# Performance work log

Hardware: AMD Instinct MI355X
Metric: run time of the kernel (lower is better)

## Reference

```python
import jax, jax.numpy as jnp
import numpy as np

S, B, H = 512, 256, 500


def setup_inputs() -> dict:
    key = jax.random.key(0)
    k1, k2, k3, k4, k5 = jax.random.split(key, 5)
    return {
        "hidden": jax.random.normal(k1, (1, B, H), dtype=jnp.float32),
        "encoder_output": jax.random.normal(k2, (S, B, H), dtype=jnp.float32),
        "W_attn": jax.random.normal(k3, (H, 2 * H), dtype=jnp.float32) * 0.02,
        "b_attn": jax.random.normal(k4, (H,), dtype=jnp.float32) * 0.02,
        "v": jax.random.normal(k5, (H,), dtype=jnp.float32),
    }


def reference(hidden, encoder_output, W_attn, b_attn, v):
    # hidden: [1, B, H] -> broadcast to [S, B, H]; concat -> [S, B, 2H]
    s, b, h = encoder_output.shape
    h_exp = jnp.broadcast_to(hidden, (s, b, h))
    cat = jnp.concatenate([h_exp, encoder_output], axis=2)  # [S, B, 2H]
    # Linear(2H -> H) with torch convention W: [out, in], then tanh
    energy = jnp.tanh(jnp.einsum("sbi,hi->sbh", cat, W_attn) + b_attn)  # [S, B, H]
    scores = jnp.einsum("sbh,h->sb", energy, v)  # [S, B]
    attn = jax.nn.softmax(scores.T, axis=1)  # [B, S]
    return attn[:, None, :]  # [B, 1, S]
```

## Files before the change

### kernel.cpp

```cpp
#include <hip/hip_runtime.h>
#include <hip/hip_fp16.h>

#define S_DIM 512
#define B_DIM 256
#define H_DIM 500
#define M_DIM (S_DIM * B_DIM)

typedef _Float16 half8_t __attribute__((ext_vector_type(8)));
typedef float    f32x4  __attribute__((ext_vector_type(4)));

#define WS_W2I 0
#define WS_AT  (512 * 1024)
#define WS_VP  (1024 * 1024)
#define WS_SC  (1024 * 1024 + 4096)

__device__ __forceinline__ void gld_lds16(const void* g, void* l) {
    __builtin_amdgcn_global_load_lds(
        (const __attribute__((address_space(1))) unsigned int*)g,
        (__attribute__((address_space(3))) unsigned int*)l, 16, 0, 0);
}

__global__ void prep_w2_v(const float* __restrict__ W, const float* __restrict__ v,
                          _Float16* __restrict__ W2i, float* __restrict__ vp) {
    int idx = blockIdx.x * blockDim.x + threadIdx.x;
#pragma unroll
    for (int r = 0; r < 2; ++r) {
        int e = idx + r * 131072;
        int n = e >> 9, k = e & 511;
        float val = (n < H_DIM && k < H_DIM) ? W[n * 1000 + 500 + k] : 0.0f;
        int nb = n >> 8, nl = n & 255, ks = k >> 5, ce = (k >> 3) & 3, u = k & 7;
        int cL = ce ^ ((nl >> 1) & 3);
        W2i[((ks * 2 + nb) * 1024 + nl * 4 + cL) * 8 + u] = (_Float16)val;
    }
    if (idx < 512) vp[idx] = (idx < H_DIM) ? v[idx] : 0.0f;
}

__global__ void prep_A(const float* __restrict__ hidden, const float* __restrict__ W,
                       const float* __restrict__ b_attn, float* __restrict__ At) {
    int b = blockIdx.x;
    int t = threadIdx.x;
    __shared__ float hs[512];
    hs[t] = (t < H_DIM) ? hidden[b * H_DIM + t] : 0.0f;
    __syncthreads();
    float acc = 0.0f;
    if (t < H_DIM) {
        acc = b_attn[t];
        const float4* wr = (const float4*)(W + t * 1000);
        const float4* hr = (const float4*)hs;
#pragma unroll 5
        for (int i = 0; i < 125; ++i) {
            float4 w4 = wr[i], h4 = hr[i];
            acc += w4.x * h4.x + w4.y * h4.y + w4.z * h4.z + w4.w * h4.w;
        }
    }
    At[t * B_DIM + b] = acc;
}

__launch_bounds__(512, 4)
__global__ void fused_attn_gemm(const float* __restrict__ enc,
                                const _Float16* __restrict__ W2i,
                                const float* __restrict__ At,
                                const float* __restrict__ vp,
                                float* __restrict__ sct) {
    __shared__ _Float16 As[2][128][32];
    __shared__ _Float16 Bs[2][256][32];
    __shared__ float    red[4][128];

    const int tid  = threadIdx.x;
    const int lane = tid & 63;
    const int wid  = tid >> 6;
    const int wm   = wid >> 2;
    const int wn   = wid & 3;
    const int l15  = lane & 15;
    const int lq   = lane >> 4;

    const int wg    = (blockIdx.x & 7) * 256 + (blockIdx.x >> 3);
    const int mblk  = wg >> 1;
    const int nblk  = wg & 1;
    const int m0    = mblk * 128;
    const int s_idx = mblk >> 1;
    const int bloc  = (mblk & 1) * 128;
    const int n0    = nblk * 256;

    const int r = tid >> 2;
    const int c = tid & 3;
    const float* gA = enc + (size_t)(m0 + r) * H_DIM + c * 8;
    const int ca = (c ^ ((r >> 1) & 3)) * 8;

    const int rch = (lq ^ ((l15 >> 1) & 3)) * 8;

    f32x4 a0, a1;

    auto ldA = [&](int slice) {
        if (slice < 15) {
            a0 = *(const f32x4*)(gA + slice * 32);
            a1 = *(const f32x4*)(gA + slice * 32 + 4);
        } else {
            const float* gr = enc + (size_t)(m0 + r) * H_DIM;
#pragma unroll
            for (int u = 0; u < 4; ++u) {
                int k0 = 480 + c * 8 + u;
                int k1 = k0 + 4;
                a0[u] = (k0 < H_DIM) ? gr[k0] : 0.0f;
                a1[u] = (k1 < H_DIM) ? gr[k1] : 0.0f;
            }
        }
    };
    auto wrA = [&](int buf) {
        half8_t h;
#pragma unroll
        for (int u = 0; u < 4; ++u) { h[u] = (_Float16)a0[u]; h[u + 4] = (_Float16)a1[u]; }
        *(half8_t*)&As[buf][r][ca] = h;
    };
    auto stB = [&](int buf, int ks) {
        const _Float16* pb = W2i + (size_t)(ks * 2 + nblk) * 8192;
        _Float16* dl = (_Float16*)&Bs[buf][0][0] + (size_t)wid * 512;
        gld_lds16(pb + (size_t)tid * 8, dl);
        gld_lds16(pb + (size_t)(tid + 512) * 8, dl + 4096);
    };

    f32x4 acc[4][4];
#pragma unroll
    for (int a = 0; a < 4; ++a)
#pragma unroll
        for (int b = 0; b < 4; ++b) acc[a][b] = 0;

    stB(0, 0);
    ldA(0);
    wrA(0);

    for (int ks = 0; ks < 16; ++ks) {
        const int cur = ks & 1;
        __syncthreads();
        if (ks < 15) {
            stB(cur ^ 1, ks + 1);
            ldA(ks + 1);
        }
        half8_t af[4], bf[4];
#pragma unroll
        for (int mf = 0; mf < 4; ++mf)
            af[mf] = *(const half8_t*)&As[cur][wm * 64 + mf * 16 + l15][rch];
#pragma unroll
        for (int nf = 0; nf < 4; ++nf)
            bf[nf] = *(const half8_t*)&Bs[cur][wn * 64 + nf * 16 + l15][rch];
#pragma unroll
        for (int mf = 0; mf < 4; ++mf)
#pragma unroll
            for (int nf = 0; nf < 4; ++nf)
                acc[mf][nf] = __builtin_amdgcn_mfma_f32_16x16x32_f16(af[mf], bf[nf], acc[mf][nf], 0, 0, 0);
        if (ks < 15) wrA(cur ^ 1);
    }

    float vpv[4];
#pragma unroll
    for (int nf = 0; nf < 4; ++nf) vpv[nf] = vp[n0 + wn * 64 + nf * 16 + l15];

    float pj[4][4];
#pragma unroll
    for (int mf = 0; mf < 4; ++mf)
#pragma unroll
        for (int j = 0; j < 4; ++j) pj[mf][j] = 0.0f;

#pragma unroll
    for (int mf = 0; mf < 4; ++mf) {
#pragma unroll
        for (int nf = 0; nf < 4; ++nf) {
            int h = n0 + wn * 64 + nf * 16 + l15;
            f32x4 av = *(const f32x4*)(At + h * B_DIM + bloc + wm * 64 + mf * 16 + lq * 4);
#pragma unroll
            for (int j = 0; j < 4; ++j) {
                float x  = acc[mf][nf][j] + av[j];
                float xc = fminf(fmaxf(x, -9.0f), 9.0f);
                float e  = __expf(2.0f * xc);
                float th = (e - 1.0f) / (e + 1.0f);
                pj[mf][j] += vpv[nf] * th;
            }
        }
    }

#pragma unroll
    for (int mf = 0; mf < 4; ++mf)
#pragma unroll
        for (int j = 0; j < 4; ++j) {
            float s = pj[mf][j];
            s += __shfl_xor(s, 1); s += __shfl_xor(s, 2);
            s += __shfl_xor(s, 4); s += __shfl_xor(s, 8);
            if (l15 == 0) red[wn][wm * 64 + mf * 16 + lq * 4 + j] = s;
        }
    __syncthreads();
    if (tid < 128) {
        float p = red[0][tid] + red[1][tid] + red[2][tid] + red[3][tid];
        sct[(size_t)nblk * M_DIM + (size_t)(bloc + tid) * S_DIM + s_idx] = p;
    }
}

__global__ void softmax_rows(const float* __restrict__ sct, float* __restrict__ out) {
    int b = blockIdx.x;
    int t = threadIdx.x;
    int lane = t & 63, w = t >> 6;
    size_t idx = (size_t)b * S_DIM + t;
    float v = sct[idx] + sct[idx + M_DIM];
    float m = v;
#pragma unroll
    for (int off = 1; off < 64; off <<= 1) m = fmaxf(m, __shfl_xor(m, off));
    __shared__ float sm[8], ss[8];
    if (lane == 0) sm[w] = m;
    __syncthreads();
    m = sm[0];
#pragma unroll
    for (int i = 1; i < 8; ++i) m = fmaxf(m, sm[i]);
    float e = __expf(v - m);
    float s = e;
#pragma unroll
    for (int off = 1; off < 64; off <<= 1) s += __shfl_xor(s, off);
    if (lane == 0) ss[w] = s;
    __syncthreads();
    s = ss[0];
#pragma unroll
    for (int i = 1; i < 8; ++i) s += ss[i];
    out[(size_t)b * S_DIM + t] = e / s;
}

extern "C" void kernel_launch(void* const* d_in, const int* in_sizes, int n_in,
                              void* d_out, int out_size, void* d_ws, size_t ws_size,
                              hipStream_t stream) {
    const float* hidden = (const float*)d_in[0];
    const float* enc    = (const float*)d_in[1];
    const float* W      = (const float*)d_in[2];
    const float* b_attn = (const float*)d_in[3];
    const float* v      = (const float*)d_in[4];
    float* out = (float*)d_out;

    char* ws = (char*)d_ws;
    _Float16* W2i = (_Float16*)(ws + WS_W2I);
    float*    At  = (float*)(ws + WS_AT);
    float*    vp  = (float*)(ws + WS_VP);
    float*    sct = (float*)(ws + WS_SC);

    prep_w2_v<<<512, 256, 0, stream>>>(W, v, W2i, vp);
    prep_A<<<256, 512, 0, stream>>>(hidden, W, b_attn, At);
    fused_attn_gemm<<<2048, 512, 0, stream>>>(enc, W2i, At, vp, sct);
    softmax_rows<<<256, 512, 0, stream>>>(sct, out);
}
```

Before: 222.6 us.

## Shrink GEMM tile to 128x128 with 256-thread blocks and four N-splits

Result: slower. 266.0 us (+19.5%).

```diff
diff --git a/kernel.cpp b/kernel.cpp
--- a/kernel.cpp
+++ b/kernel.cpp
@@ -28,9 +28,9 @@
         int e = idx + r * 131072;
         int n = e >> 9, k = e & 511;
         float val = (n < H_DIM && k < H_DIM) ? W[n * 1000 + 500 + k] : 0.0f;
-        int nb = n >> 8, nl = n & 255, ks = k >> 5, ce = (k >> 3) & 3, u = k & 7;
+        int nb = n >> 7, nl = n & 127, ks = k >> 5, ce = (k >> 3) & 3, u = k & 7;
         int cL = ce ^ ((nl >> 1) & 3);
-        W2i[((ks * 2 + nb) * 1024 + nl * 4 + cL) * 8 + u] = (_Float16)val;
+        W2i[(((ks * 4 + nb) * 512) + nl * 4 + cL) * 8 + u] = (_Float16)val;
     }
     if (idx < 512) vp[idx] = (idx < H_DIM) ? v[idx] : 0.0f;
 }
@@ -56,67 +56,73 @@
     At[t * B_DIM + b] = acc;
 }
 
-__launch_bounds__(512, 4)
+__launch_bounds__(256)
 __global__ void fused_attn_gemm(const float* __restrict__ enc,
                                 const _Float16* __restrict__ W2i,
                                 const float* __restrict__ At,
                                 const float* __restrict__ vp,
                                 float* __restrict__ sct) {
     __shared__ _Float16 As[2][128][32];
-    __shared__ _Float16 Bs[2][256][32];
-    __shared__ float    red[4][128];
+    __shared__ _Float16 Bs[2][128][32];
+    __shared__ float    red[2][128];
 
     const int tid  = threadIdx.x;
     const int lane = tid & 63;
     const int wid  = tid >> 6;
-    const int wm   = wid >> 2;
-    const int wn   = wid & 3;
+    const int wm   = wid >> 1;
+    const int wn   = wid & 1;
     const int l15  = lane & 15;
     const int lq   = lane >> 4;
 
-    const int wg    = (blockIdx.x & 7) * 256 + (blockIdx.x >> 3);
-    const int mblk  = wg >> 1;
-    const int nblk  = wg & 1;
+    const int wg    = (blockIdx.x & 7) * 512 + (blockIdx.x >> 3);
+    const int mblk  = wg >> 2;
+    const int nblk  = wg & 3;
     const int m0    = mblk * 128;
+    const int n0    = nblk * 128;
     const int s_idx = mblk >> 1;
     const int bloc  = (mblk & 1) * 128;
-    const int n0    = nblk * 256;
 
     const int r = tid >> 2;
     const int c = tid & 3;
-    const float* gA = enc + (size_t)(m0 + r) * H_DIM + c * 8;
-    const int ca = (c ^ ((r >> 1) & 3)) * 8;
+    const float* gA0 = enc + (size_t)(m0 + r) * H_DIM;
+    const float* gA1 = enc + (size_t)(m0 + 64 + r) * H_DIM;
+    const int aoff = (c ^ ((r >> 1) & 3)) * 8;
 
     const int rch = (lq ^ ((l15 >> 1) & 3)) * 8;
 
-    f32x4 a0, a1;
-
+    f32x4 a00, a01, a10, a11;
     auto ldA = [&](int slice) {
         if (slice < 15) {
-            a0 = *(const f32x4*)(gA + slice * 32);
-            a1 = *(const f32x4*)(gA + slice * 32 + 4);
+            int kb = slice * 32 + c * 8;
+            a00 = *(const f32x4*)(gA0 + kb); a01 = *(const f32x4*)(gA0 + kb + 4);
+            a10 = *(const f32x4*)(gA1 + kb); a11 = *(const f32x4*)(gA1 + kb + 4);
         } else {
-            const float* gr = enc + (size_t)(m0 + r) * H_DIM;
 #pragma unroll
             for (int u = 0; u < 4; ++u) {
-                int k0 = 480 + c * 8 + u;
-                int k1 = k0 + 4;
-                a0[u] = (k0 < H_DIM) ? gr[k0] : 0.0f;
-                a1[u] = (k1 < H_DIM) ? gr[k1] : 0.0f;
+                int k0 = 480 + c * 8 + u, k1 = k0 + 4;
+                a00[u] = (k0 < H_DIM) ? gA0[k0] : 0.0f;
+                a01[u] = (k1 < H_DIM) ? gA0[k1] : 0.0f;
+                a10[u] = (k0 < H_DIM) ? gA1[k0] : 0.0f;
+                a11[u] = (k1 < H_DIM) ? gA1[k1] : 0.0f;
             }
         }
     };
     auto wrA = [&](int buf) {
-        half8_t h;
-#pragma unroll
-        for (int u = 0; u < 4; ++u) { h[u] = (_Float16)a0[u]; h[u + 4] = (_Float16)a1[u]; }
-        *(half8_t*)&As[buf][r][ca] = h;
+        half8_t h0, h1;
+#pragma unroll
+        for (int u = 0; u < 4; ++u) {
+            h0[u] = (_Float16)a00[u]; h0[u + 4] = (_Float16)a01[u];
+            h1[u] = (_Float16)a10[u]; h1[u + 4] = (_Float16)a11[u];
+        }
+        *(half8_t*)&As[buf][r][aoff]      = h0;
+        *(half8_t*)&As[buf][64 + r][aoff] = h1;
     };
     auto stB = [&](int buf, int ks) {
-        const _Float16* pb = W2i + (size_t)(ks * 2 + nblk) * 8192;
-        _Float16* dl = (_Float16*)&Bs[buf][0][0] + (size_t)wid * 512;
-        gld_lds16(pb + (size_t)tid * 8, dl);
-        gld_lds16(pb + (size_t)(tid + 512) * 8, dl + 4096);
+        const _Float16* pb = W2i + (size_t)(ks * 4 + nblk) * 4096;
+        _Float16* dl = (_Float16*)&Bs[buf][0][0];
+        const int s0 = wid * 64, s1 = 256 + wid * 64;
+        gld_lds16(pb + (size_t)(s0 + lane) * 8, dl + s0 * 8);
+        gld_lds16(pb + (size_t)(s1 + lane) * 8, dl + s1 * 8);
     };
 
     f32x4 acc[4][4];
@@ -189,7 +195,7 @@
         }
     __syncthreads();
     if (tid < 128) {
-        float p = red[0][tid] + red[1][tid] + red[2][tid] + red[3][tid];
+        float p = red[0][tid] + red[1][tid];
         sct[(size_t)nblk * M_DIM + (size_t)(bloc + tid) * S_DIM + s_idx] = p;
     }
 }
@@ -199,7 +205,7 @@
     int t = threadIdx.x;
     int lane = t & 63, w = t >> 6;
     size_t idx = (size_t)b * S_DIM + t;
-    float v = sct[idx] + sct[idx + M_DIM];
+    float v = sct[idx] + sct[idx + M_DIM] + sct[idx + 2 * M_DIM] + sct[idx + 3 * M_DIM];
     float m = v;
 #pragma unroll
     for (int off = 1; off < 64; off <<= 1) m = fmaxf(m, __shfl_xor(m, off));
@@ -239,6 +245,6 @@
 
     prep_w2_v<<<512, 256, 0, stream>>>(W, v, W2i, vp);
     prep_A<<<256, 512, 0, stream>>>(hidden, W, b_attn, At);
-    fused_attn_gemm<<<2048, 512, 0, stream>>>(enc, W2i, At, vp, sct);
+    fused_attn_gemm<<<4096, 256, 0, stream>>>(enc, W2i, At, vp, sct);
     softmax_rows<<<256, 512, 0, stream>>>(sct, out);
 }
```
